# Performance work log

Measured on AMD Instinct MI355X. Metric: run time of the kernel, lower is better.

## Reference

```python
import jax, jax.numpy as jnp
import numpy as np

H, D, DM, L, B = 16, 64, 1024, 256, 64
SCALE = 1.0 / np.sqrt(D)   # 1/sqrt(d_head)
CHUNK = 64
LN_EPS = 1e-5


def setup_inputs() -> dict:
    key = jax.random.key(0)
    k0, k1, k2, k3 = jax.random.split(key, 4)
    h = jax.random.normal(k0, (L, B, DM), jnp.float32)
    qkv_w = jax.random.normal(k1, (H * 4 * D, DM), jnp.float32) * 0.02
    o_w = jax.random.normal(k2, (DM, H * D), jnp.float32) * 0.02
    ln_gamma = jnp.ones((DM,), jnp.float32)
    ln_beta = jnp.zeros((DM,), jnp.float32)
    pi0 = jax.random.uniform(k3, (H, 256), jnp.float32)
    return {"h": h, "qkv_w": qkv_w, "o_w": o_w,
            "ln_gamma": ln_gamma, "ln_beta": ln_beta, "pi0": pi0}


def _phi(x):
    # elu(x) + 1, then sum-normalize over feature dim
    e = jax.nn.elu(x) + 1.0
    return e / e.sum(-1, keepdims=True)


def _fast_weight_sum(q, k, v):
    # q,k,v: [B,H,L,D]. out[t] = q_t @ W_t, W_t = sum_{s<=t} k_s v_s^T (inclusive).
    # Chunked-recurrent form: intra-chunk causal GEMM + inter-chunk carried state.
    Bb, Hh, Ll, Dd = q.shape
    nc = Ll // CHUNK
    rs = lambda x: x.reshape(Bb, Hh, nc, CHUNK, Dd).transpose(2, 0, 1, 3, 4)  # [nc,B,H,C,D]
    qc, kc, vc = rs(q), rs(k), rs(v)
    mask = jnp.tril(jnp.ones((CHUNK, CHUNK), q.dtype))  # inclusive causal

    def step(W, xs):
        qi, ki, vi = xs  # [B,H,C,D]
        scores = jnp.einsum('bhtd,bhsd->bhts', qi, ki) * mask
        out = jnp.einsum('bhts,bhsd->bhtd', scores, vi) \
            + jnp.einsum('bhtd,bhde->bhte', qi, W)
        W = W + jnp.einsum('bhsd,bhse->bhde', ki, vi)
        return W, out

    W0 = jnp.zeros((Bb, Hh, Dd, Dd), q.dtype)
    _, outs = jax.lax.scan(step, W0, (qc, kc, vc))  # outs: [nc,B,H,C,D]
    return outs.transpose(1, 2, 0, 3, 4).reshape(Bb, Hh, Ll, Dd)


def reference(h, qkv_w, o_w, ln_gamma, ln_beta, pi0):
    slen, bsz, _ = h.shape
    # qkv projection and head split (rbf2keys: q, k1, k2, v)
    qkv = (h @ qkv_w.T).reshape(slen, bsz, H, 4 * D)
    hq, hk1, hk2, hv = jnp.split(qkv, 4, axis=-1)       # each [L,B,H,D]
    perm = lambda x: x.transpose(1, 2, 0, 3)            # -> [B,H,L,D]
    hq, hk1, hk2, hv = perm(hq), perm(hk1), perm(hk2), perm(hv)

    hq = _phi(hq)
    hk1 = _phi(hk1)
    hk2 = _phi(hk2)

    out1 = _fast_weight_sum(hq, hk1, hv)
    out2 = _fast_weight_sum(hq, hk2, hv)

    # skip_attn_normalization=True path: pi0-gated mixture of the two memories
    p = jnp.clip(pi0, 0.0, 1.0)[None, :, :slen, None]   # [1,H,L,1]
    layer_out = SCALE * (out1 * p + out2 * (1.0 - p))   # [B,H,L,D]

    # [B,H,L,D] -> [L,B,H*D]
    layer_out = layer_out.transpose(0, 2, 1, 3).reshape(bsz, slen, H * D).transpose(1, 0, 2)
    attn_out = layer_out @ o_w.T                        # [L,B,DM]

    # post-LN residual (pre_lnorm=False)
    x = h + attn_out
    mu = x.mean(-1, keepdims=True)
    var = ((x - mu) ** 2).mean(-1, keepdims=True)
    return (x - mu) / jnp.sqrt(var + LN_EPS) * ln_gamma + ln_beta
```

## Files before the change

### kernel.cpp

```cpp
#include <hip/hip_runtime.h>
#include <type_traits>


typedef short v8s __attribute__((ext_vector_type(8)));
typedef float v4f __attribute__((ext_vector_type(4)));

__device__ __forceinline__ float bf2f(short s) {
    unsigned int u = ((unsigned int)(unsigned short)s) << 16;
    float f;
    __builtin_memcpy(&f, &u, 4);
    return f;
}
__device__ __forceinline__ short f2bf(float f) {
    unsigned int u;
    __builtin_memcpy(&u, &f, 4);
    u = u + 0x7fffu + ((u >> 16) & 1u);
    return (short)(u >> 16);
}

__device__ __forceinline__ void load_lds16(const short* g, short* l) {
    __builtin_amdgcn_global_load_lds((const __attribute__((address_space(1))) void*)g,
                                     (__attribute__((address_space(3))) void*)l, 16, 0, 0);
}

__global__ void __launch_bounds__(256)
cvt_bf16(const float* __restrict__ in, short* __restrict__ out, int n4) {
    int i = blockIdx.x * 256 + threadIdx.x;
    if (i >= n4) return;
    float4 v = ((const float4*)in)[i];
    short4 o;
    o.x = f2bf(v.x); o.y = f2bf(v.y); o.z = f2bf(v.z); o.w = f2bf(v.w);
    ((short4*)out)[i] = o;
}

template <typename OutT>
__global__ void __launch_bounds__(512, 2)
gemm_nt(const short* __restrict__ Ap, const short* __restrict__ Bp,
        OutT* __restrict__ C, int M, int N, int K) {
    __shared__ __align__(16) short lds[2][2][256 * 64];

    const int tid = threadIdx.x;
    const int w = tid >> 6, lane = tid & 63;
    const int wm = w >> 2, wn = w & 3;
    const int lq = lane >> 4, lr = lane & 15;
    const int asw = (lr & 7) * 8;
    const int rr = tid >> 3;
    const int scol = ((tid & 7) * 8) ^ ((rr & 7) * 8);

    int bid = blockIdx.y * gridDim.x + blockIdx.x;
    int bm, bn;
    if (gridDim.x == 64) {
        int xcd = bid & 7, u = bid >> 3;
        bm = xcd * 8 + (u & 7);
        bn = u >> 3;
    } else {
        int nwg = gridDim.x * gridDim.y;
        int swz = (bid & 7) * (nwg >> 3) + (bid >> 3);
        bm = swz % gridDim.x; bn = swz / gridDim.x;
    }

    v4f acc[8][4] = {};
    v8s a[4][2];
    v8s b[2][2][2];

    const int NT = K >> 6;
    const int nIter = NT >> 1;

#define BAR_() do { asm volatile("" ::: "memory"); __builtin_amdgcn_s_barrier(); asm volatile("" ::: "memory"); } while (0)
#define SBAR_() __builtin_amdgcn_sched_barrier(0)
#define VMCNT4_() asm volatile("s_waitcnt vmcnt(4)" ::: "memory")
#define STAGE_(MAT, BUF, HALF, KT) do { \
        const short* g_ = ((MAT) ? Bp : Ap) + \
            (long)(((MAT) ? bn : bm) * 256 + (HALF) * 128 + rr) * K + (KT) * 64 + scol; \
        short* l_ = &lds[BUF][MAT][(HALF) * 8192] + w * 512; \
        load_lds16(g_, l_); \
        load_lds16(g_ + (long)64 * K, l_ + 4096); \
    } while (0)
#define LDA_(QM, BUF) do { \
        _Pragma("unroll") \
        for (int mi = 0; mi < 4; ++mi) { \
            const short* pa_ = &lds[BUF][0][(wm * 128 + (QM) * 64 + mi * 16 + lr) * 64]; \
            a[mi][0] = *(const v8s*)&pa_[(lq * 8) ^ asw]; \
            a[mi][1] = *(const v8s*)&pa_[(32 + lq * 8) ^ asw]; \
        } \
    } while (0)
#define LDB_(QN, BUF) do { \
        _Pragma("unroll") \
        for (int ni = 0; ni < 2; ++ni) { \
            const short* pb_ = &lds[BUF][1][(wn * 64 + (QN) * 32 + ni * 16 + lr) * 64]; \
            b[QN][ni][0] = *(const v8s*)&pb_[(lq * 8) ^ asw]; \
            b[QN][ni][1] = *(const v8s*)&pb_[(32 + lq * 8) ^ asw]; \
        } \
    } while (0)
#define MFMA_(QM, QN) do { \
        __builtin_amdgcn_s_setprio(1); \
        _Pragma("unroll") \
        for (int kk = 0; kk < 2; ++kk) \
            _Pragma("unroll") \
            for (int mi = 0; mi < 4; ++mi) \
                _Pragma("unroll") \
                for (int ni = 0; ni < 2; ++ni) \
                    acc[(QM) * 4 + mi][(QN) * 2 + ni] = __builtin_amdgcn_mfma_f32_16x16x32_bf16( \
                        a[mi][kk], b[QN][ni][kk], acc[(QM) * 4 + mi][(QN) * 2 + ni], 0, 0, 0); \
        __builtin_amdgcn_s_setprio(0); \
    } while (0)

    STAGE_(1, 0, 0, 0);
    STAGE_(1, 0, 1, 0);
    STAGE_(0, 0, 0, 0);
    STAGE_(0, 0, 1, 0);
    STAGE_(1, 1, 0, 1);
    STAGE_(1, 1, 1, 1);
    VMCNT4_();
    BAR_();

    for (int it = 0; it < nIter; ++it) {
        const int t1 = 2 * it + 1;
        int t2 = 2 * it + 2; if (t2 >= NT) t2 -= NT;
        int t3 = 2 * it + 3; if (t3 >= NT) t3 -= NT;

        LDA_(0, 0); LDB_(0, 0); LDB_(1, 0);
        STAGE_(0, 1, 0, t1);
        MFMA_(0, 0);
        SBAR_(); BAR_();
        STAGE_(0, 1, 1, t1);
        MFMA_(0, 1);
        SBAR_();
        LDA_(1, 0);
        SBAR_(); BAR_();
        STAGE_(1, 0, 0, t2);
        MFMA_(1, 0);
        SBAR_(); BAR_();
        STAGE_(1, 0, 1, t2);
        VMCNT4_();
        MFMA_(1, 1);
        SBAR_(); BAR_();
        LDA_(0, 1); LDB_(0, 1); LDB_(1, 1);
        STAGE_(0, 0, 0, t2);
        MFMA_(0, 0);
        SBAR_(); BAR_();
        STAGE_(0, 0, 1, t2);
        MFMA_(0, 1);
        SBAR_();
        LDA_(1, 1);
        SBAR_(); BAR_();
        STAGE_(1, 1, 0, t3);
        MFMA_(1, 0);
        SBAR_(); BAR_();
        STAGE_(1, 1, 1, t3);
        VMCNT4_();
        MFMA_(1, 1);
        SBAR_(); BAR_();
    }

#undef BAR_
#undef SBAR_
#undef VMCNT4_
#undef STAGE_
#undef LDA_
#undef LDB_
#undef MFMA_

#pragma unroll
    for (int m = 0; m < 8; ++m)
#pragma unroll
        for (int n = 0; n < 4; ++n)
#pragma unroll
            for (int r = 0; r < 4; ++r) {
                int row = bm * 256 + wm * 128 + m * 16 + lq * 4 + r;
                int col = bn * 256 + wn * 64 + n * 16 + lr;
                float v = acc[m][n][r];
                if constexpr (std::is_same_v<OutT, short>)
                    C[(long)row * N + col] = f2bf(v);
                else
                    C[(long)row * N + col] = v;
            }
}

#define SW(row, s) (((row) << 6) + ((s) ^ (((((row) >> 4) ^ (row)) & 7) << 3)))

union FW16 { int4 v[2]; short s[16]; };

__device__ __forceinline__ void phi_to_lds(const FW16& u, short* sS, short* sT,
                                           int r, int seg) {
    float f[16]; float ssum = 0.f;
#pragma unroll
    for (int i = 0; i < 16; i++) {
        float x = bf2f(u.s[i]);
        float e = x > 0.f ? x + 1.f : __expf(x);
        f[i] = e; ssum += e;
    }
    ssum += __shfl_xor(ssum, 1, 64);
    ssum += __shfl_xor(ssum, 2, 64);
    float inv = 1.f / ssum;
    FW16 o;
#pragma unroll
    for (int i = 0; i < 16; i++) o.s[i] = f2bf(f[i] * inv);
    *(int4*)&sS[SW(r, seg)] = o.v[0];
    *(int4*)&sS[SW(r, seg + 8)] = o.v[1];
    if (sT) {
#pragma unroll
        for (int i = 0; i < 16; i++) sT[SW(seg + i, r)] = o.s[i];
    }
}

__global__ void __launch_bounds__(256, 2)
fastweight(const short* __restrict__ qkv, const float* __restrict__ pi0,
           short* __restrict__ outm) {
    const int bid = blockIdx.x;
    const int h = bid & 15, b = bid >> 4;
    const int tid = threadIdx.x;
    const int w = tid >> 6, lane = tid & 63;
    const int lq = lane >> 4, lr = lane & 15;
    __shared__ __align__(16) short sq[64 * 64];
    __shared__ __align__(16) short sk1S[64 * 64];
    __shared__ __align__(16) short sk2S[64 * 64];
    __shared__ __align__(16) short sk1T[64 * 64];
    __shared__ __align__(16) short sk2T[64 * 64];
    __shared__ __align__(16) short svT[64 * 64];
    __shared__ __align__(16) short sW1T[64 * 64];
    __shared__ __align__(16) short sW2T[64 * 64];
    __shared__ float spi[256];

    for (int i = tid; i < 2048; i += 256) { ((int*)sW1T)[i] = 0; ((int*)sW2T)[i] = 0; }
    spi[tid] = pi0[h * 256 + tid];

    const int r = tid >> 2, seg = (tid & 3) * 16;

    v4f wacc1[4] = {}, wacc2[4] = {};

    FW16 cq, ck1, ck2, cv;
    {
        const short* g = qkv + ((long)(r * 64 + b)) * 4096 + h * 256 + seg;
        cq.v[0]  = *(const int4*)(g);        cq.v[1]  = *(const int4*)(g + 8);
        ck1.v[0] = *(const int4*)(g + 64);   ck1.v[1] = *(const int4*)(g + 72);
        ck2.v[0] = *(const int4*)(g + 128);  ck2.v[1] = *(const int4*)(g + 136);
        cv.v[0]  = *(const int4*)(g + 192);  cv.v[1]  = *(const int4*)(g + 200);
    }

#pragma unroll
    for (int c = 0; c < 4; c++) {
        FW16 nq, nk1, nk2, nv;
        if (c < 3) {
            const short* g = qkv + ((long)(((c + 1) * 64 + r) * 64 + b)) * 4096 + h * 256 + seg;
            nq.v[0]  = *(const int4*)(g);        nq.v[1]  = *(const int4*)(g + 8);
            nk1.v[0] = *(const int4*)(g + 64);   nk1.v[1] = *(const int4*)(g + 72);
            nk2.v[0] = *(const int4*)(g + 128);  nk2.v[1] = *(const int4*)(g + 136);
            nv.v[0]  = *(const int4*)(g + 192);  nv.v[1]  = *(const int4*)(g + 200);
        }
        __syncthreads();
        phi_to_lds(cq, sq, nullptr, r, seg);
        phi_to_lds(ck1, sk1S, sk1T, r, seg);
        phi_to_lds(ck2, sk2S, sk2T, r, seg);
#pragma unroll
        for (int i = 0; i < 16; i++) svT[SW(seg + i, r)] = cv.s[i];
        __syncthreads();

        v8s qa0 = *(const v8s*)&sq[SW(16 * w + lr, lq * 8)];
        v8s qa1 = *(const v8s*)&sq[SW(16 * w + lr, 32 + lq * 8)];

        v4f sacc1[4], sacc2[4];
#pragma unroll
        for (int n = 0; n < 4; n++) {
            v8s b10 = *(const v8s*)&sk1S[SW(16 * n + lr, lq * 8)];
            v8s b11 = *(const v8s*)&sk1S[SW(16 * n + lr, 32 + lq * 8)];
            v8s b20 = *(const v8s*)&sk2S[SW(16 * n + lr, lq * 8)];
            v8s b21 = *(const v8s*)&sk2S[SW(16 * n + lr, 32 + lq * 8)];
            v4f t1 = {}, t2 = {};
            t1 = __builtin_amdgcn_mfma_f32_16x16x32_bf16(qa0, b10, t1, 0, 0, 0);
            t2 = __builtin_amdgcn_mfma_f32_16x16x32_bf16(qa0, b20, t2, 0, 0, 0);
            t1 = __builtin_amdgcn_mfma_f32_16x16x32_bf16(qa1, b11, t1, 0, 0, 0);
            t2 = __builtin_amdgcn_mfma_f32_16x16x32_bf16(qa1, b21, t2, 0, 0, 0);
            sacc1[n] = t1; sacc2[n] = t2;
        }
        __syncthreads();
#pragma unroll
        for (int n = 0; n < 4; n++)
#pragma unroll
            for (int rr = 0; rr < 4; rr++) {
                int t_ = 16 * w + lq * 4 + rr;
                int s_ = 16 * n + lr;
                sk1S[SW(t_, s_)] = f2bf(s_ <= t_ ? sacc1[n][rr] : 0.f);
                sk2S[SW(t_, s_)] = f2bf(s_ <= t_ ? sacc2[n][rr] : 0.f);
            }

        v8s sa10 = *(const v8s*)&sk1S[SW(16 * w + lr, lq * 8)];
        v8s sa11 = *(const v8s*)&sk1S[SW(16 * w + lr, 32 + lq * 8)];
        v8s sa20 = *(const v8s*)&sk2S[SW(16 * w + lr, lq * 8)];
        v8s sa21 = *(const v8s*)&sk2S[SW(16 * w + lr, 32 + lq * 8)];
        v4f o1[4], o2[4];
#pragma unroll
        for (int n = 0; n < 4; n++) {
            v8s vb0 = *(const v8s*)&svT[SW(16 * n + lr, lq * 8)];
            v8s vb1 = *(const v8s*)&svT[SW(16 * n + lr, 32 + lq * 8)];
            v8s wb10 = *(const v8s*)&sW1T[SW(16 * n + lr, lq * 8)];
            v8s wb11 = *(const v8s*)&sW1T[SW(16 * n + lr, 32 + lq * 8)];
            v8s wb20 = *(const v8s*)&sW2T[SW(16 * n + lr, lq * 8)];
            v8s wb21 = *(const v8s*)&sW2T[SW(16 * n + lr, 32 + lq * 8)];
            v4f t1 = {}, t2 = {};
            t1 = __builtin_amdgcn_mfma_f32_16x16x32_bf16(sa10, vb0, t1, 0, 0, 0);
            t2 = __builtin_amdgcn_mfma_f32_16x16x32_bf16(sa20, vb0, t2, 0, 0, 0);
            t1 = __builtin_amdgcn_mfma_f32_16x16x32_bf16(sa11, vb1, t1, 0, 0, 0);
            t2 = __builtin_amdgcn_mfma_f32_16x16x32_bf16(sa21, vb1, t2, 0, 0, 0);
            t1 = __builtin_amdgcn_mfma_f32_16x16x32_bf16(qa0, wb10, t1, 0, 0, 0);
            t2 = __builtin_amdgcn_mfma_f32_16x16x32_bf16(qa0, wb20, t2, 0, 0, 0);
            t1 = __builtin_amdgcn_mfma_f32_16x16x32_bf16(qa1, wb11, t1, 0, 0, 0);
            t2 = __builtin_amdgcn_mfma_f32_16x16x32_bf16(qa1, wb21, t2, 0, 0, 0);
            o1[n] = t1; o2[n] = t2;
        }
#pragma unroll
        for (int n = 0; n < 4; n++)
#pragma unroll
            for (int rr = 0; rr < 4; rr++) {
                int t_ = 16 * w + lq * 4 + rr;
                int l = c * 64 + t_;
                float p = fminf(fmaxf(spi[l], 0.f), 1.f);
                float val = 0.125f * (p * o1[n][rr] + (1.f - p) * o2[n][rr]);
                long o = ((long)(l * 64 + b)) * 1024 + h * 64 + 16 * n + lr;
                outm[o] = f2bf(val);
            }

        if (c < 3) {
            __syncthreads();
            v8s va0 = *(const v8s*)&svT[SW(16 * w + lr, lq * 8)];
            v8s va1 = *(const v8s*)&svT[SW(16 * w + lr, 32 + lq * 8)];
#pragma unroll
            for (int n = 0; n < 4; n++) {
                v8s kb10 = *(const v8s*)&sk1T[SW(16 * n + lr, lq * 8)];
                v8s kb11 = *(const v8s*)&sk1T[SW(16 * n + lr, 32 + lq * 8)];
                v8s kb20 = *(const v8s*)&sk2T[SW(16 * n + lr, lq * 8)];
                v8s kb21 = *(const v8s*)&sk2T[SW(16 * n + lr, 32 + lq * 8)];
                wacc1[n] = __builtin_amdgcn_mfma_f32_16x16x32_bf16(va0, kb10, wacc1[n], 0, 0, 0);
                wacc2[n] = __builtin_amdgcn_mfma_f32_16x16x32_bf16(va0, kb20, wacc2[n], 0, 0, 0);
                wacc1[n] = __builtin_amdgcn_mfma_f32_16x16x32_bf16(va1, kb11, wacc1[n], 0, 0, 0);
                wacc2[n] = __builtin_amdgcn_mfma_f32_16x16x32_bf16(va1, kb21, wacc2[n], 0, 0, 0);
            }
#pragma unroll
            for (int n = 0; n < 4; n++)
#pragma unroll
                for (int rr = 0; rr < 4; rr++) {
                    sW1T[SW(16 * w + lq * 4 + rr, 16 * n + lr)] = f2bf(wacc1[n][rr]);
                    sW2T[SW(16 * w + lq * 4 + rr, 16 * n + lr)] = f2bf(wacc2[n][rr]);
                }
        }
        cq = nq; ck1 = nk1; ck2 = nk2; cv = nv;
    }
}

__global__ void __launch_bounds__(256)
ln_kernel(const float* __restrict__ h, const float* __restrict__ attn,
          const float* __restrict__ gamma, const float* __restrict__ beta,
          float* __restrict__ out) {
    const int row = blockIdx.x;
    const long base = (long)row * 1024;
    const int tid = threadIdx.x;
    float4 xh = ((const float4*)(h + base))[tid];
    float4 xa = ((const float4*)(attn + base))[tid];
    float4 x;
    x.x = xh.x + xa.x; x.y = xh.y + xa.y; x.z = xh.z + xa.z; x.w = xh.w + xa.w;
    float s = x.x + x.y + x.z + x.w;
    float s2 = x.x * x.x + x.y * x.y + x.z * x.z + x.w * x.w;
#pragma unroll
    for (int m = 32; m > 0; m >>= 1) {
        s += __shfl_xor(s, m, 64);
        s2 += __shfl_xor(s2, m, 64);
    }
    __shared__ float ps[4], ps2[4];
    int w = tid >> 6, lane = tid & 63;
    if (lane == 0) { ps[w] = s; ps2[w] = s2; }
    __syncthreads();
    s = ps[0] + ps[1] + ps[2] + ps[3];
    s2 = ps2[0] + ps2[1] + ps2[2] + ps2[3];
    float mu = s * (1.f / 1024.f);
    float var = s2 * (1.f / 1024.f) - mu * mu;
    float inv = rsqrtf(var + 1e-5f);
    float4 g = ((const float4*)gamma)[tid];
    float4 bb = ((const float4*)beta)[tid];
    float4 o;
    o.x = (x.x - mu) * inv * g.x + bb.x;
    o.y = (x.y - mu) * inv * g.y + bb.y;
    o.z = (x.z - mu) * inv * g.z + bb.z;
    o.w = (x.w - mu) * inv * g.w + bb.w;
    ((float4*)(out + base))[tid] = o;
}

extern "C" void kernel_launch(void* const* d_in, const int* in_sizes, int n_in,
                              void* d_out, int out_size, void* d_ws, size_t ws_size,
                              hipStream_t stream) {
    const float* h     = (const float*)d_in[0];
    const float* qkvw  = (const float*)d_in[1];
    const float* ow    = (const float*)d_in[2];
    const float* gamma = (const float*)d_in[3];
    const float* beta  = (const float*)d_in[4];
    const float* pi0   = (const float*)d_in[5];
    float* out = (float*)d_out;
    char* ws = (char*)d_ws;

    short* h_bf   = (short*)(ws);
    short* wq_bf  = (short*)(ws + 33554432);
    short* wo_bf  = (short*)(ws + 41943040);
    short* qkv_bf = (short*)(ws + 44040192);
    float* attnf  = (float*)(ws + 44040192);
    short* lmix   = h_bf;

    cvt_bf16<<<16384, 256, 0, stream>>>(h, h_bf, 16777216 / 4);
    cvt_bf16<<<4096, 256, 0, stream>>>(qkvw, wq_bf, 4194304 / 4);
    cvt_bf16<<<1024, 256, 0, stream>>>(ow, wo_bf, 1048576 / 4);

    gemm_nt<short><<<dim3(64, 16), 512, 0, stream>>>(h_bf, wq_bf, qkv_bf, 16384, 4096, 1024);

    fastweight<<<1024, 256, 0, stream>>>(qkv_bf, pi0, lmix);

    gemm_nt<float><<<dim3(64, 4), 512, 0, stream>>>(lmix, wo_bf, attnf, 16384, 1024, 1024);

    ln_kernel<<<16384, 256, 0, stream>>>(h, attnf, gamma, beta, out);
}
```

Baseline: 405.8 us.

## Restructure fastweight kernel: one wave per memory, direct-to-LDS staging

The fast-weight kernel now runs with two waves per block, and each wave owns one of the two memories (k1 or k2) across the full 64x64 chunk. The old version split rows across four waves. Q/K/V are staged into LDS with global_load_lds, with phi and the transpose applied in place, and the LDS buffers are reused for scores and the W state. This cuts LDS footprint and redundant transposes, and removes the register-held prefetch. The price is fewer threads per block and more register pressure from the 4x4 accumulator tiles. The two waves exchange their outputs through LDS before the pi-gated mix.

```diff
diff --git a/kernel.cpp b/kernel.cpp
--- a/kernel.cpp
+++ b/kernel.cpp
@@ -177,173 +177,237 @@
             }
 }
 
-#define SW(row, s) (((row) << 6) + ((s) ^ (((((row) >> 4) ^ (row)) & 7) << 3)))
-
-union FW16 { int4 v[2]; short s[16]; };
-
-__device__ __forceinline__ void phi_to_lds(const FW16& u, short* sS, short* sT,
-                                           int r, int seg) {
-    float f[16]; float ssum = 0.f;
-#pragma unroll
-    for (int i = 0; i < 16; i++) {
-        float x = bf2f(u.s[i]);
-        float e = x > 0.f ? x + 1.f : __expf(x);
-        f[i] = e; ssum += e;
-    }
-    ssum += __shfl_xor(ssum, 1, 64);
-    ssum += __shfl_xor(ssum, 2, 64);
-    float inv = 1.f / ssum;
-    FW16 o;
-#pragma unroll
-    for (int i = 0; i < 16; i++) o.s[i] = f2bf(f[i] * inv);
-    *(int4*)&sS[SW(r, seg)] = o.v[0];
-    *(int4*)&sS[SW(r, seg + 8)] = o.v[1];
-    if (sT) {
-#pragma unroll
-        for (int i = 0; i < 16; i++) sT[SW(seg + i, r)] = o.s[i];
-    }
-}
-
-__global__ void __launch_bounds__(256, 2)
+#define SZF(row, col) (((row) << 6) + ((col) ^ (((row) & 7) << 3)))
+#define LGKM0_() do { asm volatile("s_waitcnt lgkmcnt(0)" ::: "memory"); __builtin_amdgcn_sched_barrier(0); } while (0)
+
+__global__ void __launch_bounds__(128, 2)
 fastweight(const short* __restrict__ qkv, const float* __restrict__ pi0,
            short* __restrict__ outm) {
     const int bid = blockIdx.x;
     const int h = bid & 15, b = bid >> 4;
     const int tid = threadIdx.x;
-    const int w = tid >> 6, lane = tid & 63;
+    const int wv = tid >> 6, lane = tid & 63;
     const int lq = lane >> 4, lr = lane & 15;
-    __shared__ __align__(16) short sq[64 * 64];
-    __shared__ __align__(16) short sk1S[64 * 64];
-    __shared__ __align__(16) short sk2S[64 * 64];
-    __shared__ __align__(16) short sk1T[64 * 64];
-    __shared__ __align__(16) short sk2T[64 * 64];
-    __shared__ __align__(16) short svT[64 * 64];
-    __shared__ __align__(16) short sW1T[64 * 64];
-    __shared__ __align__(16) short sW2T[64 * 64];
-    __shared__ float spi[256];
-
-    for (int i = tid; i < 2048; i += 256) { ((int*)sW1T)[i] = 0; ((int*)sW2T)[i] = 0; }
-    spi[tid] = pi0[h * 256 + tid];
-
-    const int r = tid >> 2, seg = (tid & 3) * 16;
-
-    v4f wacc1[4] = {}, wacc2[4] = {};
-
-    FW16 cq, ck1, ck2, cv;
-    {
-        const short* g = qkv + ((long)(r * 64 + b)) * 4096 + h * 256 + seg;
-        cq.v[0]  = *(const int4*)(g);        cq.v[1]  = *(const int4*)(g + 8);
-        ck1.v[0] = *(const int4*)(g + 64);   ck1.v[1] = *(const int4*)(g + 72);
-        ck2.v[0] = *(const int4*)(g + 128);  ck2.v[1] = *(const int4*)(g + 136);
-        cv.v[0]  = *(const int4*)(g + 192);  cv.v[1]  = *(const int4*)(g + 200);
-    }
-
-#pragma unroll
+
+    __shared__ __align__(16) short Aq[4096];
+    __shared__ __align__(16) short Ak1[4096];
+    __shared__ __align__(16) short Ak2[4096];
+    __shared__ __align__(16) short Av[4096];
+    __shared__ __align__(16) short Aw2[4096];
+
+    short* const Akm = wv ? Ak2 : Ak1;
+    short* const Awm = wv ? Aw2 : Aq;
+
+    const int srow = lane >> 3;
+    const int scolw = ((lane & 7) ^ (srow & 7)) << 3;
+    const long LSTR = 64L * 4096;
+
+    auto stage_mat = [&](int c, int mat, short* area) {
+        const short* g = qkv + ((long)((c * 64 + srow) * 64 + b)) * 4096 + h * 256 + mat * 64 + scolw;
+#pragma unroll
+        for (int i = 0; i < 8; i++)
+            load_lds16(g + (long)i * 8 * LSTR, area + i * 512);
+    };
+
+    auto phi_inplace = [&](short* area) {
+        v8s r[8];
+#pragma unroll
+        for (int g = 0; g < 8; g++)
+            r[g] = *(const v8s*)&area[SZF(lane, g * 8)];
+        float e[64];
+        float s = 0.f;
+#pragma unroll
+        for (int g = 0; g < 8; g++)
+#pragma unroll
+            for (int k = 0; k < 8; k++) {
+                float x = bf2f(r[g][k]);
+                float v = x > 0.f ? x + 1.f : __expf(x);
+                e[g * 8 + k] = v; s += v;
+            }
+        float inv = 1.f / s;
+#pragma unroll
+        for (int g = 0; g < 8; g++) {
+            v8s o;
+#pragma unroll
+            for (int k = 0; k < 8; k++) o[k] = f2bf(e[g * 8 + k] * inv);
+            *(v8s*)&area[SZF(lane, g * 8)] = o;
+        }
+    };
+
+    auto transpose_inplace = [&](short* area) {
+        v8s r[8];
+#pragma unroll
+        for (int g = 0; g < 8; g++)
+            r[g] = *(const v8s*)&area[SZF(lane, g * 8)];
+        LGKM0_();
+#pragma unroll
+        for (int g = 0; g < 8; g++)
+#pragma unroll
+            for (int k = 0; k < 8; k++)
+                area[SZF(g * 8 + k, lane)] = r[g][k];
+    };
+
+    v4f wacc[4][4] = {};
+
+    if (wv == 0) { stage_mat(0, 0, Aq); stage_mat(0, 1, Ak1); }
+    else         { stage_mat(0, 3, Av); stage_mat(0, 2, Ak2); }
+
     for (int c = 0; c < 4; c++) {
-        FW16 nq, nk1, nk2, nv;
+        __syncthreads();
+
+        if (wv == 0) { phi_inplace(Aq); phi_inplace(Ak1); }
+        else         { transpose_inplace(Av); phi_inplace(Ak2); }
+        __syncthreads();
+
+        v8s qa[4][2], vf[4][2], kb[4][2], ktb[4][2];
+#pragma unroll
+        for (int i = 0; i < 4; i++)
+#pragma unroll
+            for (int kk = 0; kk < 2; kk++) {
+                qa[i][kk] = *(const v8s*)&Aq[SZF(16 * i + lr, 32 * kk + 8 * lq)];
+                vf[i][kk] = *(const v8s*)&Av[SZF(16 * i + lr, 32 * kk + 8 * lq)];
+                kb[i][kk] = *(const v8s*)&Akm[SZF(16 * i + lr, 32 * kk + 8 * lq)];
+            }
         if (c < 3) {
-            const short* g = qkv + ((long)(((c + 1) * 64 + r) * 64 + b)) * 4096 + h * 256 + seg;
-            nq.v[0]  = *(const int4*)(g);        nq.v[1]  = *(const int4*)(g + 8);
-            nk1.v[0] = *(const int4*)(g + 64);   nk1.v[1] = *(const int4*)(g + 72);
-            nk2.v[0] = *(const int4*)(g + 128);  nk2.v[1] = *(const int4*)(g + 136);
-            nv.v[0]  = *(const int4*)(g + 192);  nv.v[1]  = *(const int4*)(g + 200);
-        }
+#pragma unroll
+            for (int j = 0; j < 4; j++)
+#pragma unroll
+                for (int kk = 0; kk < 2; kk++) {
+                    v8s t;
+#pragma unroll
+                    for (int e = 0; e < 8; e++)
+                        t[e] = Akm[SZF(32 * kk + 8 * lq + e, 16 * j + lr)];
+                    ktb[j][kk] = t;
+                }
+        }
+
+        float pv[4][4];
+        if (wv == 0) {
+#pragma unroll
+            for (int i = 0; i < 4; i++)
+#pragma unroll
+                for (int r2 = 0; r2 < 4; r2++) {
+                    float p = pi0[h * 256 + c * 64 + 16 * i + lq * 4 + r2];
+                    pv[i][r2] = fminf(fmaxf(p, 0.f), 1.f);
+                }
+        }
+
+        unsigned int spk[4][4][2];
+#pragma unroll
+        for (int i = 0; i < 4; i++)
+#pragma unroll
+            for (int n = 0; n < 4; n++) {
+                v4f t = {};
+                t = __builtin_amdgcn_mfma_f32_16x16x32_bf16(qa[i][0], kb[n][0], t, 0, 0, 0);
+                t = __builtin_amdgcn_mfma_f32_16x16x32_bf16(qa[i][1], kb[n][1], t, 0, 0, 0);
+                unsigned int pk[2] = {0u, 0u};
+#pragma unroll
+                for (int r2 = 0; r2 < 4; r2++) {
+                    int t_ = 16 * i + lq * 4 + r2;
+                    int s_ = 16 * n + lr;
+                    unsigned int bv = (unsigned int)(unsigned short)f2bf(s_ <= t_ ? t[r2] : 0.f);
+                    pk[r2 >> 1] |= bv << (16 * (r2 & 1));
+                }
+                spk[i][n][0] = pk[0]; spk[i][n][1] = pk[1];
+            }
+
         __syncthreads();
-        phi_to_lds(cq, sq, nullptr, r, seg);
-        phi_to_lds(ck1, sk1S, sk1T, r, seg);
-        phi_to_lds(ck2, sk2S, sk2T, r, seg);
-#pragma unroll
-        for (int i = 0; i < 16; i++) svT[SW(seg + i, r)] = cv.s[i];
+
+        if (c > 0) {
+#pragma unroll
+            for (int i = 0; i < 4; i++)
+#pragma unroll
+                for (int n = 0; n < 4; n++)
+#pragma unroll
+                    for (int r2 = 0; r2 < 4; r2++)
+                        Awm[SZF(16 * i + lq * 4 + r2, 16 * n + lr)] = f2bf(wacc[i][n][r2]);
+        }
+        if (c < 3) {
+#pragma unroll
+            for (int i = 0; i < 4; i++)
+#pragma unroll
+                for (int n = 0; n < 4; n++) {
+                    wacc[i][n] = __builtin_amdgcn_mfma_f32_16x16x32_bf16(vf[i][0], ktb[n][0], wacc[i][n], 0, 0, 0);
+                    wacc[i][n] = __builtin_amdgcn_mfma_f32_16x16x32_bf16(vf[i][1], ktb[n][1], wacc[i][n], 0, 0, 0);
+                }
+        }
+#pragma unroll
+        for (int i = 0; i < 4; i++)
+#pragma unroll
+            for (int n = 0; n < 4; n++)
+#pragma unroll
+                for (int r2 = 0; r2 < 4; r2++)
+                    Akm[SZF(16 * i + lq * 4 + r2, 16 * n + lr)] =
+                        (short)(spk[i][n][r2 >> 1] >> (16 * (r2 & 1)));
+
+        LGKM0_();
+
+        v8s sa[4][2], wb[4][2];
+#pragma unroll
+        for (int i = 0; i < 4; i++)
+#pragma unroll
+            for (int kk = 0; kk < 2; kk++) {
+                sa[i][kk] = *(const v8s*)&Akm[SZF(16 * i + lr, 32 * kk + 8 * lq)];
+                if (c > 0)
+                    wb[i][kk] = *(const v8s*)&Awm[SZF(16 * i + lr, 32 * kk + 8 * lq)];
+            }
+
+        unsigned int opk[4][4][2];
+#pragma unroll
+        for (int i = 0; i < 4; i++)
+#pragma unroll
+            for (int j = 0; j < 4; j++) {
+                v4f t = {};
+                t = __builtin_amdgcn_mfma_f32_16x16x32_bf16(sa[i][0], vf[j][0], t, 0, 0, 0);
+                t = __builtin_amdgcn_mfma_f32_16x16x32_bf16(sa[i][1], vf[j][1], t, 0, 0, 0);
+                if (c > 0) {
+                    t = __builtin_amdgcn_mfma_f32_16x16x32_bf16(qa[i][0], wb[j][0], t, 0, 0, 0);
+                    t = __builtin_amdgcn_mfma_f32_16x16x32_bf16(qa[i][1], wb[j][1], t, 0, 0, 0);
+                }
+                unsigned int pk[2] = {0u, 0u};
+#pragma unroll
+                for (int r2 = 0; r2 < 4; r2++) {
+                    unsigned int bv = (unsigned int)(unsigned short)f2bf(t[r2]);
+                    pk[r2 >> 1] |= bv << (16 * (r2 & 1));
+                }
+                opk[i][j][0] = pk[0]; opk[i][j][1] = pk[1];
+            }
+
+        if (wv == 1) {
+#pragma unroll
+            for (int i = 0; i < 4; i++)
+#pragma unroll
+                for (int j = 0; j < 4; j++)
+#pragma unroll
+                    for (int r2 = 0; r2 < 4; r2++)
+                        Av[SZF(16 * i + lq * 4 + r2, 16 * j + lr)] =
+                            (short)(opk[i][j][r2 >> 1] >> (16 * (r2 & 1)));
+        }
         __syncthreads();
 
-        v8s qa0 = *(const v8s*)&sq[SW(16 * w + lr, lq * 8)];
-        v8s qa1 = *(const v8s*)&sq[SW(16 * w + lr, 32 + lq * 8)];
-
-        v4f sacc1[4], sacc2[4];
-#pragma unroll
-        for (int n = 0; n < 4; n++) {
-            v8s b10 = *(const v8s*)&sk1S[SW(16 * n + lr, lq * 8)];
-            v8s b11 = *(const v8s*)&sk1S[SW(16 * n + lr, 32 + lq * 8)];
-            v8s b20 = *(const v8s*)&sk2S[SW(16 * n + lr, lq * 8)];
-            v8s b21 = *(const v8s*)&sk2S[SW(16 * n + lr, 32 + lq * 8)];
-            v4f t1 = {}, t2 = {};
-            t1 = __builtin_amdgcn_mfma_f32_16x16x32_bf16(qa0, b10, t1, 0, 0, 0);
-            t2 = __builtin_amdgcn_mfma_f32_16x16x32_bf16(qa0, b20, t2, 0, 0, 0);
-            t1 = __builtin_amdgcn_mfma_f32_16x16x32_bf16(qa1, b11, t1, 0, 0, 0);
-            t2 = __builtin_amdgcn_mfma_f32_16x16x32_bf16(qa1, b21, t2, 0, 0, 0);
-            sacc1[n] = t1; sacc2[n] = t2;
+        if (wv == 0) {
+#pragma unroll
+            for (int i = 0; i < 4; i++)
+#pragma unroll
+                for (int j = 0; j < 4; j++)
+#pragma unroll
+                    for (int r2 = 0; r2 < 4; r2++) {
+                        int t_ = 16 * i + lq * 4 + r2;
+                        float o1 = bf2f((short)(opk[i][j][r2 >> 1] >> (16 * (r2 & 1))));
+                        float o2 = bf2f(Av[SZF(t_, 16 * j + lr)]);
+                        float p = pv[i][r2];
+                        float val = 0.125f * (p * o1 + (1.f - p) * o2);
+                        outm[((long)((c * 64 + t_) * 64 + b)) * 1024 + h * 64 + 16 * j + lr] = f2bf(val);
+                    }
+        } else if (c < 3) {
+            stage_mat(c + 1, 2, Ak2);
         }
         __syncthreads();
-#pragma unroll
-        for (int n = 0; n < 4; n++)
-#pragma unroll
-            for (int rr = 0; rr < 4; rr++) {
-                int t_ = 16 * w + lq * 4 + rr;
-                int s_ = 16 * n + lr;
-                sk1S[SW(t_, s_)] = f2bf(s_ <= t_ ? sacc1[n][rr] : 0.f);
-                sk2S[SW(t_, s_)] = f2bf(s_ <= t_ ? sacc2[n][rr] : 0.f);
-            }
-
-        v8s sa10 = *(const v8s*)&sk1S[SW(16 * w + lr, lq * 8)];
-        v8s sa11 = *(const v8s*)&sk1S[SW(16 * w + lr, 32 + lq * 8)];
-        v8s sa20 = *(const v8s*)&sk2S[SW(16 * w + lr, lq * 8)];
-        v8s sa21 = *(const v8s*)&sk2S[SW(16 * w + lr, 32 + lq * 8)];
-        v4f o1[4], o2[4];
-#pragma unroll
-        for (int n = 0; n < 4; n++) {
-            v8s vb0 = *(const v8s*)&svT[SW(16 * n + lr, lq * 8)];
-            v8s vb1 = *(const v8s*)&svT[SW(16 * n + lr, 32 + lq * 8)];
-            v8s wb10 = *(const v8s*)&sW1T[SW(16 * n + lr, lq * 8)];
-            v8s wb11 = *(const v8s*)&sW1T[SW(16 * n + lr, 32 + lq * 8)];
-            v8s wb20 = *(const v8s*)&sW2T[SW(16 * n + lr, lq * 8)];
-            v8s wb21 = *(const v8s*)&sW2T[SW(16 * n + lr, 32 + lq * 8)];
-            v4f t1 = {}, t2 = {};
-            t1 = __builtin_amdgcn_mfma_f32_16x16x32_bf16(sa10, vb0, t1, 0, 0, 0);
-            t2 = __builtin_amdgcn_mfma_f32_16x16x32_bf16(sa20, vb0, t2, 0, 0, 0);
-            t1 = __builtin_amdgcn_mfma_f32_16x16x32_bf16(sa11, vb1, t1, 0, 0, 0);
-            t2 = __builtin_amdgcn_mfma_f32_16x16x32_bf16(sa21, vb1, t2, 0, 0, 0);
-            t1 = __builtin_amdgcn_mfma_f32_16x16x32_bf16(qa0, wb10, t1, 0, 0, 0);
-            t2 = __builtin_amdgcn_mfma_f32_16x16x32_bf16(qa0, wb20, t2, 0, 0, 0);
-            t1 = __builtin_amdgcn_mfma_f32_16x16x32_bf16(qa1, wb11, t1, 0, 0, 0);
-            t2 = __builtin_amdgcn_mfma_f32_16x16x32_bf16(qa1, wb21, t2, 0, 0, 0);
-            o1[n] = t1; o2[n] = t2;
-        }
-#pragma unroll
-        for (int n = 0; n < 4; n++)
-#pragma unroll
-            for (int rr = 0; rr < 4; rr++) {
-                int t_ = 16 * w + lq * 4 + rr;
-                int l = c * 64 + t_;
-                float p = fminf(fmaxf(spi[l], 0.f), 1.f);
-                float val = 0.125f * (p * o1[n][rr] + (1.f - p) * o2[n][rr]);
-                long o = ((long)(l * 64 + b)) * 1024 + h * 64 + 16 * n + lr;
-                outm[o] = f2bf(val);
-            }
 
         if (c < 3) {
-            __syncthreads();
-            v8s va0 = *(const v8s*)&svT[SW(16 * w + lr, lq * 8)];
-            v8s va1 = *(const v8s*)&svT[SW(16 * w + lr, 32 + lq * 8)];
-#pragma unroll
-            for (int n = 0; n < 4; n++) {
-                v8s kb10 = *(const v8s*)&sk1T[SW(16 * n + lr, lq * 8)];
-                v8s kb11 = *(const v8s*)&sk1T[SW(16 * n + lr, 32 + lq * 8)];
-                v8s kb20 = *(const v8s*)&sk2T[SW(16 * n + lr, lq * 8)];
-                v8s kb21 = *(const v8s*)&sk2T[SW(16 * n + lr, 32 + lq * 8)];
-                wacc1[n] = __builtin_amdgcn_mfma_f32_16x16x32_bf16(va0, kb10, wacc1[n], 0, 0, 0);
-                wacc2[n] = __builtin_amdgcn_mfma_f32_16x16x32_bf16(va0, kb20, wacc2[n], 0, 0, 0);
-                wacc1[n] = __builtin_amdgcn_mfma_f32_16x16x32_bf16(va1, kb11, wacc1[n], 0, 0, 0);
-                wacc2[n] = __builtin_amdgcn_mfma_f32_16x16x32_bf16(va1, kb21, wacc2[n], 0, 0, 0);
-            }
-#pragma unroll
-            for (int n = 0; n < 4; n++)
-#pragma unroll
-                for (int rr = 0; rr < 4; rr++) {
-                    sW1T[SW(16 * w + lq * 4 + rr, 16 * n + lr)] = f2bf(wacc1[n][rr]);
-                    sW2T[SW(16 * w + lq * 4 + rr, 16 * n + lr)] = f2bf(wacc2[n][rr]);
-                }
-        }
-        cq = nq; ck1 = nk1; ck2 = nk2; cv = nv;
+            if (wv == 0) { stage_mat(c + 1, 0, Aq); stage_mat(c + 1, 1, Ak1); }
+            else         { stage_mat(c + 1, 3, Av); }
+        }
     }
 }
 
@@ -409,7 +473,7 @@
 
     gemm_nt<short><<<dim3(64, 16), 512, 0, stream>>>(h_bf, wq_bf, qkv_bf, 16384, 4096, 1024);
 
-    fastweight<<<1024, 256, 0, stream>>>(qkv_bf, pi0, lmix);
+    fastweight<<<1024, 128, 0, stream>>>(qkv_bf, pi0, lmix);
 
     gemm_nt<float><<<dim3(64, 4), 512, 0, stream>>>(lmix, wo_bf, attnf, 16384, 1024, 1024);
 
```

After: 682.7 us. +68.3%, slower.
